# Kernel tuning notes

Measured on AMD Instinct MI355X. Metric: run time of the kernel, lower is better.

## Reference

```python
import jax, jax.numpy as jnp
import numpy as np

ALPHA = 3.0   # self.alpha
TAU = 0.1     # contrastive temperature
K = 8         # configs.k (top-k hyperedges per node)


def _scale(x, w, ehy, enod):
    """One scale of incidence_matrix_learn.
    x: [B, L, D] series tokens; w: [ws, D] word tokens;
    ehy: [H, D] hyperedge embedding table; enod: [N, D] node embedding table, N = L + ws.
    Returns (binary incidence matrix [N, H] float32, scalar contrastive loss).
    """
    B = x.shape[0]
    # concat_all[i]: cat(x.permute(0,2,1), word_expanded) -> [B, D, N]
    we = jnp.broadcast_to(w.T[None], (B,) + w.T.shape)          # [B, D, ws]
    concat = jnp.concatenate([jnp.transpose(x, (0, 2, 1)), we], axis=-1)  # [B, D, N]
    N, H = enod.shape[0], ehy.shape[0]
    # adjacency: softmax(relu(alpha * nodeec @ hyperen.T)) along hyperedge dim
    a = enod @ ehy.T                                            # [N, H]
    adj = jax.nn.softmax(jax.nn.relu(ALPHA * a), axis=-1)
    # top-k mask + threshold > 0.5 -> binary incidence matrix
    k = min(H, K)
    _, idx = jax.lax.top_k(adj, k)                              # [N, k]
    mask = jnp.zeros_like(adj).at[jnp.arange(N)[:, None], idx].set(1.0)
    adj_bin = ((adj * mask) > 0.5).astype(jnp.float32)          # [N, H]
    # positives: nodes sharing any hyperedge (build_pos_indices_from_edge_index),
    # equivalent to (A A^T > 0) with self excluded; dropping all-zero columns is a no-op here
    P = (adj_bin @ adj_bin.T > 0) & ~jnp.eye(N, dtype=bool)     # [N, N]
    cnt = P.sum(axis=1)                                         # positives per node
    # acl_loss_batched, vectorized over batch and nodes
    nodes = jnp.transpose(concat, (0, 2, 1))                    # [B, N, D]
    nrm = nodes / jnp.maximum(jnp.linalg.norm(nodes, axis=-1, keepdims=True), 1e-12)
    sim = jnp.einsum('bnd,bmd->bnm', nrm, nrm) / TAU            # [B, N, N]
    denom = jax.nn.logsumexp(sim, axis=-1)                      # [B, N]
    pos_mean = jnp.einsum('bnm,nm->bn', sim, P.astype(sim.dtype)) / jnp.maximum(cnt, 1)
    valid = cnt > 0                                             # [N]
    loss_sum = jnp.sum(jnp.where(valid[None, :], denom - pos_mean, 0.0))
    vc = B * valid.sum()
    loss = jnp.where(vc > 0, loss_sum / jnp.maximum(vc, 1), 0.0)
    return adj_bin, loss


def setup_inputs() -> dict:
    key = jax.random.key(0)
    ks = jax.random.split(key, 8)
    B, D = 64, 512
    return dict(
        x0=jax.random.normal(ks[0], (B, 512, D), dtype=jnp.float32),
        x1=jax.random.normal(ks[1], (B, 256, D), dtype=jnp.float32),
        word0=jax.random.normal(ks[2], (128, D), dtype=jnp.float32),
        word1=jax.random.normal(ks[3], (128, D), dtype=jnp.float32),
        embhy0=jax.random.normal(ks[4], (128, D), dtype=jnp.float32),
        embhy1=jax.random.normal(ks[5], (64, D), dtype=jnp.float32),
        embnod0=jax.random.normal(ks[6], (640, D), dtype=jnp.float32),
        embnod1=jax.random.normal(ks[7], (384, D), dtype=jnp.float32),
    )


def reference(x0, x1, word0, word1, embhy0, embhy1, embnod0, embnod1):
    a0, l0 = _scale(x0, word0, embhy0, embnod0)
    a1, l1 = _scale(x1, word1, embhy1, embnod1)
    return (a0, a1, l0 + l1)
```

## Files before the change

kernel.cpp:

```cpp
#include <hip/hip_runtime.h>


#define DDIM 512
#define BATCH 64
#define NGID 65536

typedef __attribute__((ext_vector_type(8))) short short8;
typedef __attribute__((ext_vector_type(4))) float f32x4;

__constant__ int POS_SCALE[16] = {0,0,0,0, 0,1,0,0, 1,1,0,0, 0,1,1,1};
__constant__ int POS_TU[16]    = {0,1,2,3, 9,5,7,4, 0,1,5,6, 8,2,3,4};

__device__ __forceinline__ unsigned short f2bf(float f) {
  unsigned int u = __float_as_uint(f);
  u += 0x7fffu + ((u >> 16) & 1u);
  return (unsigned short)(u >> 16);
}

__device__ __forceinline__ void async16(const void* g, void* l) {
  __builtin_amdgcn_global_load_lds(
      (const __attribute__((address_space(1))) unsigned int*)g,
      (__attribute__((address_space(3))) unsigned int*)l, 16, 0, 0);
}

__device__ __forceinline__ int m3(int x) {
  x -= (x >= 6) ? 6 : 0;
  x -= (x >= 3) ? 3 : 0;
  return x;
}

__global__ __launch_bounds__(256) void prep_kernel(
    const float* __restrict__ enod0, const float* __restrict__ ehy0,
    const float* __restrict__ enod1, const float* __restrict__ ehy1,
    float* __restrict__ adj0, float* __restrict__ adj1,
    int* __restrict__ labels0, int* __restrict__ labels1,
    const float* __restrict__ x0, const float* __restrict__ w0,
    const float* __restrict__ x1, const float* __restrict__ w1,
    unsigned short* __restrict__ nhat0, unsigned short* __restrict__ nhat1,
    float* __restrict__ acc, int* __restrict__ ticket) {
  const int t = threadIdx.x;
  if (blockIdx.x < 1024) {
    if (blockIdx.x == 0 && t == 0) { acc[0] = 0.f; acc[1] = 0.f; ticket[0] = 0; }
    const bool s0 = blockIdx.x < 640;
    const int n = s0 ? blockIdx.x : blockIdx.x - 640;
    const int H = s0 ? 128 : 64;
    const float* enod = s0 ? enod0 : enod1;
    const float* ehy = s0 ? ehy0 : ehy1;
    float* out_adj = s0 ? adj0 : adj1;
    int* labels = s0 ? labels0 : labels1;
    __shared__ float erow[DDIM];
    __shared__ float red[128];
    __shared__ int lab;
    if (t < 128) ((float4*)erow)[t] = ((const float4*)(enod + (size_t)n * DDIM))[t];
    if (t == 0) lab = -1;
    __syncthreads();
    float v = 0.f;
    if (t < H) {
      const float4* hr = (const float4*)(ehy + (size_t)t * DDIM);
      float a = 0.f;
      #pragma unroll 8
      for (int d = 0; d < DDIM / 4; ++d) {
        float4 h = hr[d];
        float4 e = ((const float4*)erow)[d];
        a = fmaf(h.x, e.x, a); a = fmaf(h.y, e.y, a);
        a = fmaf(h.z, e.z, a); a = fmaf(h.w, e.w, a);
      }
      v = fmaxf(0.f, 3.0f * a);
    }
    if (t < 128) red[t] = v;
    __syncthreads();
    for (int s = 64; s > 0; s >>= 1) {
      if (t < s) red[t] = fmaxf(red[t], red[t + s]);
      __syncthreads();
    }
    const float mx = red[0];
    __syncthreads();
    const float e = (t < H) ? __expf(v - mx) : 0.f;
    if (t < 128) red[t] = e;
    __syncthreads();
    for (int s = 64; s > 0; s >>= 1) {
      if (t < s) red[t] += red[t + s];
      __syncthreads();
    }
    const float sum = red[0];
    if (t < H) {
      const float adj = e / sum;
      const float bin = (adj > 0.5f) ? 1.0f : 0.0f;
      out_adj[(size_t)n * H + t] = bin;
      if (bin > 0.f) lab = t;
    }
    __syncthreads();
    if (t == 0) labels[n] = lab;
  } else {
    const int wave = t >> 6;
    const int lane = t & 63;
    const int g = (blockIdx.x - 1024) * 4 + wave;
    const bool s0 = g < BATCH * 640;
    const int gg = s0 ? g : g - BATCH * 640;
    const int N = s0 ? 640 : 384;
    const int L = s0 ? 512 : 256;
    const float* x = s0 ? x0 : x1;
    const float* w = s0 ? w0 : w1;
    unsigned short* nhat = s0 ? nhat0 : nhat1;
    const int b = gg / N;
    const int n = gg - b * N;
    const float* src = (n < L) ? (x + ((size_t)b * L + n) * DDIM)
                               : (w + (size_t)(n - L) * DDIM);
    const float4* rowp = (const float4*)src;
    const float4 v0 = rowp[lane];
    const float4 v1 = rowp[lane + 64];
    float ss = v0.x * v0.x + v0.y * v0.y + v0.z * v0.z + v0.w * v0.w +
               v1.x * v1.x + v1.y * v1.y + v1.z * v1.z + v1.w * v1.w;
    #pragma unroll
    for (int off = 32; off > 0; off >>= 1) ss += __shfl_xor(ss, off);
    const float rinv = 1.0f / fmaxf(sqrtf(ss), 1e-12f);
    ushort4 o0, o1;
    o0.x = f2bf(v0.x * rinv); o0.y = f2bf(v0.y * rinv);
    o0.z = f2bf(v0.z * rinv); o0.w = f2bf(v0.w * rinv);
    o1.x = f2bf(v1.x * rinv); o1.y = f2bf(v1.y * rinv);
    o1.z = f2bf(v1.z * rinv); o1.w = f2bf(v1.w * rinv);
    ushort4* op = (ushort4*)(nhat + ((size_t)b * N + n) * DDIM);
    op[lane] = o0;
    op[lane + 64] = o1;
  }
}

__global__ __launch_bounds__(256) void cnt_kernel(
    const int* __restrict__ labels0, int* __restrict__ cnt0,
    const int* __restrict__ labels1, int* __restrict__ cnt1,
    int* __restrict__ valid) {
  const bool s0 = blockIdx.x == 0;
  const int* labels = s0 ? labels0 : labels1;
  int* cnt = s0 ? cnt0 : cnt1;
  int* validcnt = s0 ? valid : valid + 1;
  const int N = s0 ? 640 : 384;
  __shared__ int lab[640];
  __shared__ int hist[128];
  __shared__ int vc;
  const int t = threadIdx.x;
  if (t == 0) vc = 0;
  if (t < 128) hist[t] = 0;
  for (int i = t; i < N; i += 256) lab[i] = labels[i];
  __syncthreads();
  for (int i = t; i < N; i += 256)
    if (lab[i] >= 0) atomicAdd(&hist[lab[i]], 1);
  __syncthreads();
  int lv = 0;
  for (int i = t; i < N; i += 256) {
    const int c = (lab[i] >= 0) ? hist[lab[i]] - 1 : 0;
    cnt[i] = c;
    if (c > 0) ++lv;
  }
  if (lv > 0) atomicAdd(&vc, lv);
  __syncthreads();
  if (t == 0) *validcnt = vc;
}

__global__ __launch_bounds__(128, 2) void lse_kernel(
    const unsigned short* __restrict__ nhat0, const int* __restrict__ labels0,
    const unsigned short* __restrict__ nhat1, const int* __restrict__ labels1,
    float2* __restrict__ sp) {
  __shared__ short8 Bbuf[3][512];
  __shared__ float2 redC[2][64];
  __shared__ int labS[640];
  const int tid = threadIdx.x;
  const int pos = blockIdx.x >> 6;
  const int b = blockIdx.x & 63;
  const bool s0 = POS_SCALE[pos] == 0;
  const int tu = POS_TU[pos];
  const int nt = s0 ? 10 : 6;
  const int N = s0 ? 640 : 384;
  const unsigned short* nhat = s0 ? nhat0 : nhat1;
  const int* labels = s0 ? labels0 : labels1;
  const int gbase = s0 ? b * 640 : 40960 + b * 384;

  const int wave = tid >> 6;
  const int lane = tid & 63;
  const int lrow = lane & 15;
  const int lq = lane >> 4;

  for (int t = tid; t < N; t += 128) labS[t] = labels[t];

  const size_t base = (size_t)b * N * DDIM;
  const int rw0 = tu * 64 + wave * 32;
  const unsigned short* Ap0 = nhat + base + (size_t)(rw0 + lrow) * DDIM + lq * 8;
  const unsigned short* Ap1 = Ap0 + (size_t)16 * DDIM;
  short8 a0[16], a1[16];
  #pragma unroll
  for (int ks = 0; ks < 16; ++ks) {
    a0[ks] = *(const short8*)(Ap0 + ks * 32);
    a1[ks] = *(const short8*)(Ap1 + ks * 32);
  }

  __syncthreads();

  int labn[2][4];
  #pragma unroll
  for (int s = 0; s < 2; ++s)
    #pragma unroll
    for (int r = 0; r < 4; ++r) labn[s][r] = labS[rw0 + s * 16 + lq * 4 + r];

  const unsigned short* Bp0 = nhat + base + (size_t)tu * 64 * DDIM;
  const int f0 = wave * 4;
  #pragma unroll
  for (int pc = 0; pc < 2; ++pc) {
    #pragma unroll
    for (int fi = 0; fi < 4; ++fi) {
      const int f = f0 + fi, j = f >> 1, ks = f & 1;
      async16(Bp0 + (size_t)(j * 16 + lrow) * DDIM + pc * 64 + ks * 32 + lq * 8,
              &Bbuf[pc][f * 64]);
    }
  }

  float rSE[2][4] = {{0.f, 0.f, 0.f, 0.f}, {0.f, 0.f, 0.f, 0.f}};
  float rPOS[2][4] = {{0.f, 0.f, 0.f, 0.f}, {0.f, 0.f, 0.f, 0.f}};
  int slotb = 0;

  for (int tv = tu; tv < nt; ++tv) {
    asm volatile("" : "+v"(a0[0]), "+v"(a0[1]), "+v"(a0[2]), "+v"(a0[3]),
                      "+v"(a0[4]), "+v"(a0[5]), "+v"(a0[6]), "+v"(a0[7]));
    asm volatile("" : "+v"(a0[8]), "+v"(a0[9]), "+v"(a0[10]), "+v"(a0[11]),
                      "+v"(a0[12]), "+v"(a0[13]), "+v"(a0[14]), "+v"(a0[15]));
    asm volatile("" : "+v"(a1[0]), "+v"(a1[1]), "+v"(a1[2]), "+v"(a1[3]),
                      "+v"(a1[4]), "+v"(a1[5]), "+v"(a1[6]), "+v"(a1[7]));
    asm volatile("" : "+v"(a1[8]), "+v"(a1[9]), "+v"(a1[10]), "+v"(a1[11]),
                      "+v"(a1[12]), "+v"(a1[13]), "+v"(a1[14]), "+v"(a1[15]));
    const bool diag = (tv == tu);
    const bool last = (tv == nt - 1);
    const unsigned short* Bcur = nhat + base + (size_t)tv * 64 * DDIM;
    const unsigned short* Bnxt = Bcur + (size_t)64 * DDIM;
    const int sl[3] = {slotb, m3(slotb + 1), m3(slotb + 2)};

    f32x4 acc[4][2];
    #pragma unroll
    for (int j = 0; j < 4; ++j) {
      acc[j][0] = (f32x4){0.f, 0.f, 0.f, 0.f};
      acc[j][1] = (f32x4){0.f, 0.f, 0.f, 0.f};
    }
    #pragma unroll
    for (int kc = 0; kc < 8; ++kc) {
      if (last && kc == 7) asm volatile("s_waitcnt vmcnt(0)" ::: "memory");
      else                 asm volatile("s_waitcnt vmcnt(4)" ::: "memory");
      __builtin_amdgcn_s_barrier();
      if (!(last && kc >= 6)) {
        const unsigned short* Bsrc = (kc < 6) ? Bcur : Bnxt;
        const int kcol = (kc < 6) ? kc + 2 : kc - 6;
        short8* dst = &Bbuf[sl[(kc + 2) % 3]][0];
        #pragma unroll
        for (int fi = 0; fi < 4; ++fi) {
          const int f = f0 + fi, j = f >> 1, ks = f & 1;
          async16(Bsrc + (size_t)(j * 16 + lrow) * DDIM + kcol * 64 + ks * 32 + lq * 8,
                  dst + f * 64);
        }
      }
      const short8* bb = &Bbuf[sl[kc % 3]][0];
      #pragma unroll
      for (int ks = 0; ks < 2; ++ks) {
        const short8 b0 = bb[(0 + ks) * 64 + lane];
        const short8 b1 = bb[(2 + ks) * 64 + lane];
        const short8 b2 = bb[(4 + ks) * 64 + lane];
        const short8 b3 = bb[(6 + ks) * 64 + lane];
        const short8 av0 = a0[kc * 2 + ks];
        const short8 av1 = a1[kc * 2 + ks];
        acc[0][0] = __builtin_amdgcn_mfma_f32_16x16x32_bf16(av0, b0, acc[0][0], 0, 0, 0);
        acc[0][1] = __builtin_amdgcn_mfma_f32_16x16x32_bf16(av1, b0, acc[0][1], 0, 0, 0);
        acc[1][0] = __builtin_amdgcn_mfma_f32_16x16x32_bf16(av0, b1, acc[1][0], 0, 0, 0);
        acc[1][1] = __builtin_amdgcn_mfma_f32_16x16x32_bf16(av1, b1, acc[1][1], 0, 0, 0);
        acc[2][0] = __builtin_amdgcn_mfma_f32_16x16x32_bf16(av0, b2, acc[2][0], 0, 0, 0);
        acc[2][1] = __builtin_amdgcn_mfma_f32_16x16x32_bf16(av1, b2, acc[2][1], 0, 0, 0);
        acc[3][0] = __builtin_amdgcn_mfma_f32_16x16x32_bf16(av0, b3, acc[3][0], 0, 0, 0);
        acc[3][1] = __builtin_amdgcn_mfma_f32_16x16x32_bf16(av1, b3, acc[3][1], 0, 0, 0);
      }
    }

    float cSE[4] = {0.f, 0.f, 0.f, 0.f};
    float cPOS[4] = {0.f, 0.f, 0.f, 0.f};
    #pragma unroll
    for (int j = 0; j < 4; ++j) {
      const int v = tv * 64 + j * 16 + lrow;
      const int labm = labS[v];
      #pragma unroll
      for (int s = 0; s < 2; ++s) {
        const int u0 = rw0 + s * 16 + lq * 4;
        #pragma unroll
        for (int r = 0; r < 4; ++r) {
          const float sim = acc[j][s][r] * 10.0f;
          const float e = __expf(sim - 10.0f);
          rSE[s][r] += e;
          const bool match = (labn[s][r] >= 0) && (labm == labn[s][r]);
          if (match && v != u0 + r) rPOS[s][r] += sim;
          if (!diag) {
            cSE[j] += e;
            if (match) cPOS[j] += sim;
          }
        }
      }
    }
    if (!diag) {
      #pragma unroll
      for (int off = 16; off <= 32; off <<= 1) {
        #pragma unroll
        for (int j = 0; j < 4; ++j) {
          cSE[j] += __shfl_xor(cSE[j], off);
          cPOS[j] += __shfl_xor(cPOS[j], off);
        }
      }
      if (lane < 16) {
        #pragma unroll
        for (int j = 0; j < 4; ++j) {
          float2 st; st.x = cSE[j]; st.y = cPOS[j];
          redC[wave][j * 16 + lane] = st;
        }
      }
      asm volatile("s_waitcnt lgkmcnt(0)" ::: "memory");
      __builtin_amdgcn_s_barrier();
      if (lane < 32) {
        const int v = wave * 32 + lane;
        const float2 c0 = redC[0][v];
        const float2 c1 = redC[1][v];
        float2 st; st.x = c0.x + c1.x; st.y = c0.y + c1.y;
        sp[(size_t)(1 + tu) * NGID + gbase + tv * 64 + v] = st;
      }
    }
    slotb = m3(slotb + 2);
  }

  #pragma unroll
  for (int off = 1; off <= 8; off <<= 1) {
    #pragma unroll
    for (int s = 0; s < 2; ++s)
      #pragma unroll
      for (int r = 0; r < 4; ++r) {
        rSE[s][r] += __shfl_xor(rSE[s][r], off);
        rPOS[s][r] += __shfl_xor(rPOS[s][r], off);
      }
  }
  if (lrow == 0) {
    #pragma unroll
    for (int s = 0; s < 2; ++s)
      #pragma unroll
      for (int r = 0; r < 4; ++r) {
        const int u = rw0 + s * 16 + lq * 4 + r;
        float2 st; st.x = rSE[s][r]; st.y = rPOS[s][r];
        sp[gbase + u] = st;
      }
  }
}

__global__ __launch_bounds__(256) void loss_reduce(
    const float2* __restrict__ sp, const int* __restrict__ cnt0,
    const int* __restrict__ cnt1, float* __restrict__ acc,
    const int* __restrict__ valid, int* __restrict__ ticket,
    float* __restrict__ lossp) {
  __shared__ float r0[4], r1[4];
  const int t = threadIdx.x;
  float l0 = 0.f, l1 = 0.f;
  for (int g = blockIdx.x * 256 + t; g < NGID; g += 64 * 256) {
    const bool is0 = g < 40960;
    const int n = is0 ? (g % 640) : ((g - 40960) % 384);
    const int tb = n >> 6;
    float se = 0.f, pos = 0.f;
    for (int s = 0; s <= tb; ++s) {
      const float2 v = sp[(size_t)s * NGID + g];
      se += v.x; pos += v.y;
    }
    const int c = is0 ? cnt0[n] : cnt1[n];
    if (c > 0) {
      const float v = (10.0f + logf(se)) - pos / (float)c;
      if (is0) l0 += v; else l1 += v;
    }
  }
  #pragma unroll
  for (int off = 32; off > 0; off >>= 1) {
    l0 += __shfl_xor(l0, off);
    l1 += __shfl_xor(l1, off);
  }
  if ((t & 63) == 0) { r0[t >> 6] = l0; r1[t >> 6] = l1; }
  __syncthreads();
  if (t == 0) {
    atomicAdd(&acc[0], r0[0] + r0[1] + r0[2] + r0[3]);
    atomicAdd(&acc[1], r1[0] + r1[1] + r1[2] + r1[3]);
    __threadfence();
    const int done = atomicAdd(ticket, 1);
    if (done == 63) {
      const float a0v = atomicAdd(&acc[0], 0.0f);
      const float a1v = atomicAdd(&acc[1], 0.0f);
      float l = 0.f;
      if (valid[0] > 0) l += a0v / (float)(BATCH * valid[0]);
      if (valid[1] > 0) l += a1v / (float)(BATCH * valid[1]);
      lossp[0] = l;
    }
  }
}

extern "C" void kernel_launch(void* const* d_in, const int* in_sizes, int n_in,
                              void* d_out, int out_size, void* d_ws,
                              size_t ws_size, hipStream_t stream) {
  const float* x0 = (const float*)d_in[0];
  const float* x1 = (const float*)d_in[1];
  const float* w0 = (const float*)d_in[2];
  const float* w1 = (const float*)d_in[3];
  const float* ehy0 = (const float*)d_in[4];
  const float* ehy1 = (const float*)d_in[5];
  const float* enod0 = (const float*)d_in[6];
  const float* enod1 = (const float*)d_in[7];

  float* out = (float*)d_out;
  float* adj0 = out;
  float* adj1 = out + 640 * 128;
  float* lossp = out + 640 * 128 + 384 * 64;

  unsigned short* nhat0 = (unsigned short*)d_ws;
  unsigned short* nhat1 = nhat0 + (size_t)BATCH * 640 * DDIM;
  int* ip = (int*)(nhat1 + (size_t)BATCH * 384 * DDIM);
  int* labels0 = ip;
  int* labels1 = labels0 + 640;
  int* cnt0 = labels1 + 384;
  int* cnt1 = cnt0 + 640;
  int* valid = cnt1 + 384;
  int* ticket = valid + 2;
  float* acc = (float*)(ticket + 1);
  float2* sp = (float2*)((((size_t)(acc + 2)) + 255) & ~(size_t)255);

  prep_kernel<<<1024 + 16384, 256, 0, stream>>>(
      enod0, ehy0, enod1, ehy1, adj0, adj1, labels0, labels1,
      x0, w0, x1, w1, nhat0, nhat1, acc, ticket);
  cnt_kernel<<<2, 256, 0, stream>>>(labels0, cnt0, labels1, cnt1, valid);
  lse_kernel<<<1024, 128, 0, stream>>>(nhat0, labels0, nhat1, labels1, sp);
  loss_reduce<<<64, 256, 0, stream>>>(sp, cnt0, cnt1, acc, valid, ticket,
                                      lossp);
}
```

Measured before the change: 252.2 us.

## Retile symmetric Gram LSE kernel into 128-row bands with 8-wave blocks

The symmetric similarity tile schedule is restructured. Each block now has 8 waves and covers a 128-row band, split into two interleaved column halves that stride over the upper-triangle tiles. Each wave holds one 16-row A fragment, and each B tile staged in LDS is shared by more waves. The partial-sum slot layout and the loss_reduce slot count change to match. The aim is better load balance and more LDS reuse, at the cost of a larger block, more barriers across 8 waves, and a more complex diagonal and self-exclusion logic.

New measurement: 245.1 us. 2.8% less time.

```diff
diff --git a/kernel.cpp b/kernel.cpp
--- a/kernel.cpp
+++ b/kernel.cpp
@@ -4,12 +4,14 @@
 #define DDIM 512
 #define BATCH 64
 #define NGID 65536
+#define NSLOT 6
 
 typedef __attribute__((ext_vector_type(8))) short short8;
 typedef __attribute__((ext_vector_type(4))) float f32x4;
 
-__constant__ int POS_SCALE[16] = {0,0,0,0, 0,1,0,0, 1,1,0,0, 0,1,1,1};
-__constant__ int POS_TU[16]    = {0,1,2,3, 9,5,7,4, 0,1,5,6, 8,2,3,4};
+__constant__ int CLS_SCALE[8] = {0, 0, 0, 1, 0, 1, 0, 1};
+__constant__ int CLS_BU[8]    = {0, 1, 2, 0, 3, 1, 4, 2};
+__constant__ int CLS_NTL[8]   = {5, 4, 3, 3, 2, 2, 1, 1};
 
 __device__ __forceinline__ unsigned short f2bf(float f) {
   unsigned int u = __float_as_uint(f);
@@ -156,123 +158,110 @@
   if (t == 0) *validcnt = vc;
 }
 
-__global__ __launch_bounds__(128, 2) void lse_kernel(
+__global__ __launch_bounds__(512, 4) void lse_kernel(
     const unsigned short* __restrict__ nhat0, const int* __restrict__ labels0,
     const unsigned short* __restrict__ nhat1, const int* __restrict__ labels1,
     float2* __restrict__ sp) {
-  __shared__ short8 Bbuf[3][512];
-  __shared__ float2 redC[2][64];
+  __shared__ short8 Bbuf[3][1024];
+  __shared__ float2 redC[8][64];
   __shared__ int labS[640];
   const int tid = threadIdx.x;
-  const int pos = blockIdx.x >> 6;
+  const int cls = blockIdx.x >> 7;
+  const int half = (blockIdx.x >> 6) & 1;
   const int b = blockIdx.x & 63;
-  const bool s0 = POS_SCALE[pos] == 0;
-  const int tu = POS_TU[pos];
-  const int nt = s0 ? 10 : 6;
+  const bool s0 = CLS_SCALE[cls] == 0;
+  const int bu = CLS_BU[cls];
+  const int ntl = CLS_NTL[cls];
   const int N = s0 ? 640 : 384;
   const unsigned short* nhat = s0 ? nhat0 : nhat1;
   const int* labels = s0 ? labels0 : labels1;
   const int gbase = s0 ? b * 640 : 40960 + b * 384;
 
-  const int wave = tid >> 6;
+  const int w = tid >> 6;
   const int lane = tid & 63;
   const int lrow = lane & 15;
   const int lq = lane >> 4;
-
-  for (int t = tid; t < N; t += 128) labS[t] = labels[t];
+  const int wq = w & 3;
+  const int ut = 2 * bu + (w >> 2);
+
+  for (int t = tid; t < N; t += 512) labS[t] = labels[t];
 
   const size_t base = (size_t)b * N * DDIM;
-  const int rw0 = tu * 64 + wave * 32;
-  const unsigned short* Ap0 = nhat + base + (size_t)(rw0 + lrow) * DDIM + lq * 8;
-  const unsigned short* Ap1 = Ap0 + (size_t)16 * DDIM;
-  short8 a0[16], a1[16];
+  const int bandrow0 = bu * 128;
+  const int myrow = bandrow0 + w * 16 + lrow;
+  const unsigned short* Ap = nhat + base + (size_t)myrow * DDIM + lq * 8;
+  short8 a[16];
   #pragma unroll
-  for (int ks = 0; ks < 16; ++ks) {
-    a0[ks] = *(const short8*)(Ap0 + ks * 32);
-    a1[ks] = *(const short8*)(Ap1 + ks * 32);
-  }
+  for (int ki = 0; ki < 16; ++ki) a[ki] = *(const short8*)(Ap + ki * 32);
 
   __syncthreads();
 
-  int labn[2][4];
+  int labn[4];
   #pragma unroll
-  for (int s = 0; s < 2; ++s)
-    #pragma unroll
-    for (int r = 0; r < 4; ++r) labn[s][r] = labS[rw0 + s * 16 + lq * 4 + r];
-
-  const unsigned short* Bp0 = nhat + base + (size_t)tu * 64 * DDIM;
-  const int f0 = wave * 4;
+  for (int r = 0; r < 4; ++r)
+    labn[r] = labS[bandrow0 + w * 16 + lq * 4 + r];
+
+  const int tv0 = 2 * bu + half;
+  const unsigned short* Bp0 = nhat + base + (size_t)tv0 * 64 * DDIM;
+  const int f0 = w * 2;
   #pragma unroll
   for (int pc = 0; pc < 2; ++pc) {
     #pragma unroll
-    for (int fi = 0; fi < 4; ++fi) {
-      const int f = f0 + fi, j = f >> 1, ks = f & 1;
-      async16(Bp0 + (size_t)(j * 16 + lrow) * DDIM + pc * 64 + ks * 32 + lq * 8,
+    for (int fi = 0; fi < 2; ++fi) {
+      const int f = f0 + fi, j = f >> 2, ks = f & 3;
+      async16(Bp0 + (size_t)(j * 16 + lrow) * DDIM + pc * 128 + ks * 32 + lq * 8,
               &Bbuf[pc][f * 64]);
     }
   }
 
-  float rSE[2][4] = {{0.f, 0.f, 0.f, 0.f}, {0.f, 0.f, 0.f, 0.f}};
-  float rPOS[2][4] = {{0.f, 0.f, 0.f, 0.f}, {0.f, 0.f, 0.f, 0.f}};
+  float rSE[4] = {0.f, 0.f, 0.f, 0.f};
+  float rPOS[4] = {0.f, 0.f, 0.f, 0.f};
   int slotb = 0;
 
-  for (int tv = tu; tv < nt; ++tv) {
-    asm volatile("" : "+v"(a0[0]), "+v"(a0[1]), "+v"(a0[2]), "+v"(a0[3]),
-                      "+v"(a0[4]), "+v"(a0[5]), "+v"(a0[6]), "+v"(a0[7]));
-    asm volatile("" : "+v"(a0[8]), "+v"(a0[9]), "+v"(a0[10]), "+v"(a0[11]),
-                      "+v"(a0[12]), "+v"(a0[13]), "+v"(a0[14]), "+v"(a0[15]));
-    asm volatile("" : "+v"(a1[0]), "+v"(a1[1]), "+v"(a1[2]), "+v"(a1[3]),
-                      "+v"(a1[4]), "+v"(a1[5]), "+v"(a1[6]), "+v"(a1[7]));
-    asm volatile("" : "+v"(a1[8]), "+v"(a1[9]), "+v"(a1[10]), "+v"(a1[11]),
-                      "+v"(a1[12]), "+v"(a1[13]), "+v"(a1[14]), "+v"(a1[15]));
-    const bool diag = (tv == tu);
-    const bool last = (tv == nt - 1);
+  for (int ti = 0; ti < ntl; ++ti) {
+    const int tv = tv0 + 2 * ti;
+    const bool last = (ti == ntl - 1);
     const unsigned short* Bcur = nhat + base + (size_t)tv * 64 * DDIM;
-    const unsigned short* Bnxt = Bcur + (size_t)64 * DDIM;
+    const unsigned short* Bnxt = Bcur + (size_t)128 * DDIM;
     const int sl[3] = {slotb, m3(slotb + 1), m3(slotb + 2)};
 
-    f32x4 acc[4][2];
-    #pragma unroll
-    for (int j = 0; j < 4; ++j) {
-      acc[j][0] = (f32x4){0.f, 0.f, 0.f, 0.f};
-      acc[j][1] = (f32x4){0.f, 0.f, 0.f, 0.f};
-    }
-    #pragma unroll
-    for (int kc = 0; kc < 8; ++kc) {
-      if (last && kc == 7) asm volatile("s_waitcnt vmcnt(0)" ::: "memory");
-      else                 asm volatile("s_waitcnt vmcnt(4)" ::: "memory");
+    f32x4 acc[4];
+    #pragma unroll
+    for (int j = 0; j < 4; ++j) acc[j] = (f32x4){0.f, 0.f, 0.f, 0.f};
+
+    #pragma unroll
+    for (int kc = 0; kc < 4; ++kc) {
+      if (last && kc == 3) asm volatile("s_waitcnt vmcnt(0)" ::: "memory");
+      else                 asm volatile("s_waitcnt vmcnt(2)" ::: "memory");
       __builtin_amdgcn_s_barrier();
-      if (!(last && kc >= 6)) {
-        const unsigned short* Bsrc = (kc < 6) ? Bcur : Bnxt;
-        const int kcol = (kc < 6) ? kc + 2 : kc - 6;
+      if (!(last && kc >= 2)) {
+        const unsigned short* Bsrc = (kc < 2) ? Bcur : Bnxt;
+        const int kcol = (kc + 2) & 3;
         short8* dst = &Bbuf[sl[(kc + 2) % 3]][0];
         #pragma unroll
-        for (int fi = 0; fi < 4; ++fi) {
-          const int f = f0 + fi, j = f >> 1, ks = f & 1;
-          async16(Bsrc + (size_t)(j * 16 + lrow) * DDIM + kcol * 64 + ks * 32 + lq * 8,
+        for (int fi = 0; fi < 2; ++fi) {
+          const int f = f0 + fi, j = f >> 2, ks = f & 3;
+          async16(Bsrc + (size_t)(j * 16 + lrow) * DDIM + kcol * 128 + ks * 32 + lq * 8,
                   dst + f * 64);
         }
       }
       const short8* bb = &Bbuf[sl[kc % 3]][0];
       #pragma unroll
-      for (int ks = 0; ks < 2; ++ks) {
-        const short8 b0 = bb[(0 + ks) * 64 + lane];
-        const short8 b1 = bb[(2 + ks) * 64 + lane];
-        const short8 b2 = bb[(4 + ks) * 64 + lane];
-        const short8 b3 = bb[(6 + ks) * 64 + lane];
-        const short8 av0 = a0[kc * 2 + ks];
-        const short8 av1 = a1[kc * 2 + ks];
-        acc[0][0] = __builtin_amdgcn_mfma_f32_16x16x32_bf16(av0, b0, acc[0][0], 0, 0, 0);
-        acc[0][1] = __builtin_amdgcn_mfma_f32_16x16x32_bf16(av1, b0, acc[0][1], 0, 0, 0);
-        acc[1][0] = __builtin_amdgcn_mfma_f32_16x16x32_bf16(av0, b1, acc[1][0], 0, 0, 0);
-        acc[1][1] = __builtin_amdgcn_mfma_f32_16x16x32_bf16(av1, b1, acc[1][1], 0, 0, 0);
-        acc[2][0] = __builtin_amdgcn_mfma_f32_16x16x32_bf16(av0, b2, acc[2][0], 0, 0, 0);
-        acc[2][1] = __builtin_amdgcn_mfma_f32_16x16x32_bf16(av1, b2, acc[2][1], 0, 0, 0);
-        acc[3][0] = __builtin_amdgcn_mfma_f32_16x16x32_bf16(av0, b3, acc[3][0], 0, 0, 0);
-        acc[3][1] = __builtin_amdgcn_mfma_f32_16x16x32_bf16(av1, b3, acc[3][1], 0, 0, 0);
-      }
-    }
-
+      for (int ks = 0; ks < 4; ++ks) {
+        const short8 b0 = bb[(0 * 4 + ks) * 64 + lane];
+        const short8 b1 = bb[(1 * 4 + ks) * 64 + lane];
+        const short8 b2 = bb[(2 * 4 + ks) * 64 + lane];
+        const short8 b3 = bb[(3 * 4 + ks) * 64 + lane];
+        const short8 av = a[kc * 4 + ks];
+        acc[0] = __builtin_amdgcn_mfma_f32_16x16x32_bf16(av, b0, acc[0], 0, 0, 0);
+        acc[1] = __builtin_amdgcn_mfma_f32_16x16x32_bf16(av, b1, acc[1], 0, 0, 0);
+        acc[2] = __builtin_amdgcn_mfma_f32_16x16x32_bf16(av, b2, acc[2], 0, 0, 0);
+        acc[3] = __builtin_amdgcn_mfma_f32_16x16x32_bf16(av, b3, acc[3], 0, 0, 0);
+      }
+    }
+
+    const bool diag = (ut == tv);
+    const bool colp = (tv >= 2 * bu + 2);
     float cSE[4] = {0.f, 0.f, 0.f, 0.f};
     float cPOS[4] = {0.f, 0.f, 0.f, 0.f};
     #pragma unroll
@@ -280,23 +269,20 @@
       const int v = tv * 64 + j * 16 + lrow;
       const int labm = labS[v];
       #pragma unroll
-      for (int s = 0; s < 2; ++s) {
-        const int u0 = rw0 + s * 16 + lq * 4;
-        #pragma unroll
-        for (int r = 0; r < 4; ++r) {
-          const float sim = acc[j][s][r] * 10.0f;
-          const float e = __expf(sim - 10.0f);
-          rSE[s][r] += e;
-          const bool match = (labn[s][r] >= 0) && (labm == labn[s][r]);
-          if (match && v != u0 + r) rPOS[s][r] += sim;
-          if (!diag) {
-            cSE[j] += e;
-            if (match) cPOS[j] += sim;
-          }
+      for (int r = 0; r < 4; ++r) {
+        const float sim = acc[j][r] * 10.0f;
+        const float e = __expf(sim - 10.0f);
+        rSE[r] += e;
+        const bool match = (labn[r] >= 0) && (labm == labn[r]);
+        const bool self = diag && (j == wq) && (lrow == lq * 4 + r);
+        if (match && !self) rPOS[r] += sim;
+        if (colp) {
+          cSE[j] += e;
+          if (match) cPOS[j] += sim;
         }
       }
     }
-    if (!diag) {
+    if (colp) {
       #pragma unroll
       for (int off = 16; off <= 32; off <<= 1) {
         #pragma unroll
@@ -309,41 +295,40 @@
         #pragma unroll
         for (int j = 0; j < 4; ++j) {
           float2 st; st.x = cSE[j]; st.y = cPOS[j];
-          redC[wave][j * 16 + lane] = st;
+          redC[w][j * 16 + lane] = st;
         }
       }
       asm volatile("s_waitcnt lgkmcnt(0)" ::: "memory");
       __builtin_amdgcn_s_barrier();
-      if (lane < 32) {
-        const int v = wave * 32 + lane;
-        const float2 c0 = redC[0][v];
-        const float2 c1 = redC[1][v];
-        float2 st; st.x = c0.x + c1.x; st.y = c0.y + c1.y;
-        sp[(size_t)(1 + tu) * NGID + gbase + tv * 64 + v] = st;
-      }
-    }
-    slotb = m3(slotb + 2);
+      if (tid < 64) {
+        float se = 0.f, ps = 0.f;
+        #pragma unroll
+        for (int ww = 0; ww < 8; ++ww) {
+          const float2 c = redC[ww][tid];
+          se += c.x; ps += c.y;
+        }
+        float2 st; st.x = se; st.y = ps;
+        sp[(size_t)(2 + bu) * NGID + gbase + tv * 64 + tid] = st;
+      }
+    }
+    slotb = m3(slotb + 1);
   }
 
   #pragma unroll
   for (int off = 1; off <= 8; off <<= 1) {
     #pragma unroll
-    for (int s = 0; s < 2; ++s)
-      #pragma unroll
-      for (int r = 0; r < 4; ++r) {
-        rSE[s][r] += __shfl_xor(rSE[s][r], off);
-        rPOS[s][r] += __shfl_xor(rPOS[s][r], off);
-      }
+    for (int r = 0; r < 4; ++r) {
+      rSE[r] += __shfl_xor(rSE[r], off);
+      rPOS[r] += __shfl_xor(rPOS[r], off);
+    }
   }
   if (lrow == 0) {
     #pragma unroll
-    for (int s = 0; s < 2; ++s)
-      #pragma unroll
-      for (int r = 0; r < 4; ++r) {
-        const int u = rw0 + s * 16 + lq * 4 + r;
-        float2 st; st.x = rSE[s][r]; st.y = rPOS[s][r];
-        sp[gbase + u] = st;
-      }
+    for (int r = 0; r < 4; ++r) {
+      const int u = bandrow0 + w * 16 + lq * 4 + r;
+      float2 st; st.x = rSE[r]; st.y = rPOS[r];
+      sp[(size_t)half * NGID + gbase + u] = st;
+    }
   }
 }
 
@@ -358,9 +343,10 @@
   for (int g = blockIdx.x * 256 + t; g < NGID; g += 64 * 256) {
     const bool is0 = g < 40960;
     const int n = is0 ? (g % 640) : ((g - 40960) % 384);
-    const int tb = n >> 6;
+    const int tt = n >> 6;
+    const int nslots = 2 + (tt >> 1);
     float se = 0.f, pos = 0.f;
-    for (int s = 0; s <= tb; ++s) {
+    for (int s = 0; s < nslots; ++s) {
       const float2 v = sp[(size_t)s * NGID + g];
       se += v.x; pos += v.y;
     }
@@ -426,7 +412,7 @@
       enod0, ehy0, enod1, ehy1, adj0, adj1, labels0, labels1,
       x0, w0, x1, w1, nhat0, nhat1, acc, ticket);
   cnt_kernel<<<2, 256, 0, stream>>>(labels0, cnt0, labels1, cnt1, valid);
-  lse_kernel<<<1024, 128, 0, stream>>>(nhat0, labels0, nhat1, labels1, sp);
+  lse_kernel<<<1024, 512, 0, stream>>>(nhat0, labels0, nhat1, labels1, sp);
   loss_reduce<<<64, 256, 0, stream>>>(sp, cnt0, cnt1, acc, valid, ticket,
                                       lossp);
 }
```
